# Kernel tuning notes

Measured on AMD Instinct MI355X. Metric: run time of the kernel, lower is better.

## Reference

```python
import jax, jax.numpy as jnp
import numpy as np


def setup_inputs() -> dict:
    key = jax.random.key(0)
    k1, k2, k3 = jax.random.split(key, 3)
    B, V, J = 32, 100000, 52
    vertices = jax.random.normal(k1, (1, V, 3), dtype=jnp.float32)
    lbs_weights = jax.random.uniform(k2, (1, V, J), dtype=jnp.float32)
    skinning_transforms = jax.random.normal(k3, (B, J, 4, 4), dtype=jnp.float32)
    return {
        "vertices": vertices,
        "lbs_weights": lbs_weights,
        "skinning_transforms": skinning_transforms,
    }


def reference(vertices, lbs_weights, skinning_transforms):
    # 3D-vertices branch of Skinning.forward
    B = skinning_transforms.shape[0]
    J = skinning_transforms.shape[1]
    V = vertices.shape[1]
    # W: [B,V,J] (broadcast of [1,V,J]); T_flat: [B,V,16] -> T: [B,V,4,4]
    T = jnp.einsum(
        "bvj,bjx->bvx",
        jnp.broadcast_to(lbs_weights, (B, V, J)),
        skinning_transforms.reshape(B, J, 16),
    ).reshape(B, V, 4, 4)
    # homogeneous vertex coords [B,V,4]
    v_posed_homo = jnp.concatenate(
        [
            jnp.broadcast_to(vertices, (B, V, 3)),
            jnp.ones((B, V, 1), dtype=vertices.dtype),
        ],
        axis=2,
    )
    # per-vertex 4x4 @ 4 transform, keep xyz
    v_homo = jnp.einsum("bvij,bvj->bvi", T, v_posed_homo)
    return v_homo[:, :, :3]
```

## Files before the change

kernel.cpp:

```cpp
#include <hip/hip_runtime.h>
#include <hip/hip_bf16.h>


typedef __attribute__((ext_vector_type(8))) short bf16x8;
typedef __attribute__((ext_vector_type(4))) float f32x4;

constexpr int J      = 52;
constexpr int KSTEPS = 7;
constexpr int NT     = 6;
constexpr int WAVES  = 4;
constexpr int MT     = 2;
constexpr int VPW    = MT * 16;
constexpr int VPB    = WAVES * VPW;

constexpr int SLOTS_FULL = 6 * NT * 64;
constexpr int SLOTS_S6   = NT * 32;
constexpr int ZSLOT      = SLOTS_FULL + SLOTS_S6;
constexpr int NSLOT      = ZSLOT + 1;
constexpr int S6_BASE_B  = SLOTS_FULL * 16;
constexpr int Z_B        = ZSLOT * 16;
constexpr int LDS_B      = 40960;
constexpr int SL_B       = 16 * VPW * 3 * 4;

typedef const __attribute__((address_space(1))) char* gas1_t;
typedef __attribute__((address_space(3))) char* las3_t;

__device__ __forceinline__ unsigned pk2(float a, float b) {
    __hip_bfloat162 h = __float22bfloat162_rn(make_float2(a, b));
    return *reinterpret_cast<unsigned*>(&h);
}

__global__ __launch_bounds__(256) void pack_A(
    const float* __restrict__ xf,
    bf16x8* __restrict__ Bp)
{
    const int slot = blockIdx.x * 256 + threadIdx.x;
    if (slot >= NSLOT) return;

    if (slot == ZSLOT) {
        union { bf16x8 v; unsigned w[4]; } z;
        z.w[0] = z.w[1] = z.w[2] = z.w[3] = 0u;
        Bp[slot] = z.v;
        return;
    }

    int s, t, l;
    if (slot < SLOTS_FULL) {
        s = slot / (NT * 64);
        const int rem = slot - s * (NT * 64);
        t = rem >> 6;
        l = rem & 63;
    } else {
        s = 6;
        const int rem = slot - SLOTS_FULL;
        t = rem >> 5;
        l = rem & 31;
    }
    const int lgrp = l >> 4;
    const int lrow = l & 15;
    const int n = t * 16 + lrow;
    const int b = n / 3;
    const int i = n - 3 * b;
    const int j0 = s * 8 + lgrp * 2;

    const float4* __restrict__ xf4 = reinterpret_cast<const float4*>(xf);
    const float4 m0 = xf4[(b * J + j0) * 4 + i];
    const float4 m1 = xf4[(b * J + j0 + 1) * 4 + i];
    union { bf16x8 v; unsigned w[4]; } r;
    r.w[0] = pk2(m0.x, m0.y); r.w[1] = pk2(m0.z, m0.w);
    r.w[2] = pk2(m1.x, m1.y); r.w[3] = pk2(m1.z, m1.w);
    Bp[slot] = r.v;
}

__global__ __launch_bounds__(256, 4) void skin_mfma(
    const float* __restrict__ verts,
    const float* __restrict__ weights,
    const bf16x8* __restrict__ Bp,
    float* __restrict__ out,
    int V)
{
    __shared__ __align__(16) char sBp[LDS_B];

    const int tid  = threadIdx.x;
    const int lane = tid & 63;
    const int wid  = tid >> 6;
    const int lgrp = lane >> 4;
    const int lrow = lane & 15;
    const int v0   = blockIdx.x * VPB;
    const int v0w  = v0 + wid * VPW;

    {
        const char* g = (const char*)Bp;
        for (int p = wid; p < LDS_B / 1024; p += WAVES) {
            __builtin_amdgcn_global_load_lds(
                (gas1_t)(g + p * 1024 + lane * 16),
                (las3_t)(sBp + p * 1024), 16, 0, 0);
        }
    }

    float hx[MT], hy[MT], hz[MT];
    float2 wv[MT][KSTEPS];
#pragma unroll
    for (int mt = 0; mt < MT; ++mt) {
        const int v   = v0w + mt * 16 + lrow;
        const int vcl = (v < V) ? v : (V - 1);
        hx[mt] = verts[3 * (size_t)vcl + 0];
        hy[mt] = verts[3 * (size_t)vcl + 1];
        hz[mt] = verts[3 * (size_t)vcl + 2];
        const float* wr = weights + (size_t)vcl * J;
#pragma unroll
        for (int s = 0; s < KSTEPS; ++s) {
            const int j0 = s * 8 + lgrp * 2;
            wv[mt][s] = (j0 < J) ? *(const float2*)(wr + j0) : float2{0.f, 0.f};
        }
    }

    __syncthreads();

    f32x4 acc[MT][NT];
#pragma unroll
    for (int mt = 0; mt < MT; ++mt)
#pragma unroll
        for (int t = 0; t < NT; ++t)
            acc[mt][t] = f32x4{0.f, 0.f, 0.f, 0.f};

#pragma unroll
    for (int s = 0; s < KSTEPS; ++s) {
        bf16x8 frag[NT];
#pragma unroll
        for (int t = 0; t < NT; ++t) {
            if (s < 6) {
                frag[t] = *(const bf16x8*)(sBp + ((s * NT + t) * 64 + lane) * 16);
            } else {
                const char* p = (lane < 32)
                    ? (sBp + S6_BASE_B + (t * 32 + lane) * 16)
                    : (sBp + Z_B);
                frag[t] = *(const bf16x8*)p;
            }
        }
#pragma unroll
        for (int mt = 0; mt < MT; ++mt) {
            const float w0 = wv[mt][s].x, w1 = wv[mt][s].y;
            union { bf16x8 v; unsigned w[4]; } xf8;
            xf8.w[0] = pk2(w0 * hx[mt], w0 * hy[mt]);
            xf8.w[1] = pk2(w0 * hz[mt], w0);
            xf8.w[2] = pk2(w1 * hx[mt], w1 * hy[mt]);
            xf8.w[3] = pk2(w1 * hz[mt], w1);
#pragma unroll
            for (int t = 0; t < NT; ++t) {
                acc[mt][t] = __builtin_amdgcn_mfma_f32_16x16x32_bf16(
                    frag[t], xf8.v, acc[mt][t], 0, 0, 0);
            }
        }
    }

    __syncthreads();

    char* const sl = sBp + wid * SL_B;
    const long long validf = ((long long)V - v0w) * 3;
#pragma unroll
    for (int h = 0; h < 2; ++h) {
#pragma unroll
        for (int mt = 0; mt < MT; ++mt) {
            const int vloc = mt * 16 + lrow;
#pragma unroll
            for (int tt = 0; tt < 3; ++tt) {
                const int t = 3 * h + tt;
#pragma unroll
                for (int r = 0; r < 4; ++r) {
                    const int n  = 16 * t + lgrp * 4 + r;
                    const int b  = n / 3;
                    const int i  = n - 3 * b;
                    const int fl = ((b - 16 * h) * VPW + vloc) * 3 + i;
                    *(float*)(sl + fl * 4) = acc[mt][t][r];
                }
            }
        }
        asm volatile("s_waitcnt lgkmcnt(0)" ::: "memory");
        __builtin_amdgcn_sched_barrier(0);

        f32x4 vals[6];
#pragma unroll
        for (int q = 0; q < 6; ++q) {
            const int f = q * 64 + lane;
            vals[q] = *(const f32x4*)(sl + f * 16);
        }
        asm volatile("s_waitcnt lgkmcnt(0)" ::: "memory");
        __builtin_amdgcn_sched_barrier(0);

#pragma unroll
        for (int q = 0; q < 6; ++q) {
            const int f  = q * 64 + lane;
            const int bl = f / 24;
            const int rr = f - bl * 24;
            float* dst = out + (size_t)(16 * h + bl) * (size_t)V * 3
                             + (size_t)v0w * 3 + rr * 4;
            if ((long long)(rr + 1) * 4 <= validf) {
                *(float4*)dst = *(const float4*)&vals[q];
            } else if ((long long)rr * 4 < validf) {
#pragma unroll
                for (int e = 0; e < 4; ++e)
                    if ((long long)(rr * 4 + e) < validf) dst[e] = vals[q][e];
            }
        }
    }
}

extern "C" void kernel_launch(void* const* d_in, const int* in_sizes, int n_in,
                              void* d_out, int out_size, void* d_ws, size_t ws_size,
                              hipStream_t stream)
{
    const float* verts   = (const float*)d_in[0];
    const float* weights = (const float*)d_in[1];
    const float* xf      = (const float*)d_in[2];
    float* out = (float*)d_out;

    const int V = in_sizes[0] / 3;
    bf16x8* Bp = (bf16x8*)d_ws;

    pack_A<<<(NSLOT + 255) / 256, 256, 0, stream>>>(xf, Bp);
    const int nblocks = (V + VPB - 1) / VPB;
    skin_mfma<<<nblocks, 256, 0, stream>>>(verts, weights, Bp, out, V);
}
```

Baseline: 23.84 us.

## Split LDS staging of packed transforms and pad epilogue scratch rows

The LDS fill of packed transform fragments is split in two. Only the first three K-steps' data is awaited before compute starts, and the remainder loads asynchronously while the first MFMA steps run, with an extra barrier before the later steps. The epilogue scratch layout is also padded from 96 to 100 floats per batch row to reduce LDS bank conflicts on the transposing stores. This adds a barrier and changes LDS addressing, and the padded scratch region per wave grows to 6400 bytes, which still fits within the LDS buffer.

```diff
diff --git a/kernel.cpp b/kernel.cpp
--- a/kernel.cpp
+++ b/kernel.cpp
@@ -6,12 +6,12 @@
 typedef __attribute__((ext_vector_type(4))) float f32x4;
 
 constexpr int J      = 52;
-constexpr int KSTEPS = 7;
 constexpr int NT     = 6;
 constexpr int WAVES  = 4;
 constexpr int MT     = 2;
 constexpr int VPW    = MT * 16;
 constexpr int VPB    = WAVES * VPW;
+constexpr int KSTEPS = 7;
 
 constexpr int SLOTS_FULL = 6 * NT * 64;
 constexpr int SLOTS_S6   = NT * 32;
@@ -20,7 +20,9 @@
 constexpr int S6_BASE_B  = SLOTS_FULL * 16;
 constexpr int Z_B        = ZSLOT * 16;
 constexpr int LDS_B      = 40960;
-constexpr int SL_B       = 16 * VPW * 3 * 4;
+constexpr int H1_B       = 3 * NT * 64 * 16;
+constexpr int SPAD       = 100;
+constexpr int SL_B       = 16 * SPAD * 4;
 
 typedef const __attribute__((address_space(1))) char* gas1_t;
 typedef __attribute__((address_space(3))) char* las3_t;
@@ -91,7 +93,7 @@
 
     {
         const char* g = (const char*)Bp;
-        for (int p = wid; p < LDS_B / 1024; p += WAVES) {
+        for (int p = wid; p < H1_B / 1024; p += WAVES) {
             __builtin_amdgcn_global_load_lds(
                 (gas1_t)(g + p * 1024 + lane * 16),
                 (las3_t)(sBp + p * 1024), 16, 0, 0);
@@ -117,6 +119,15 @@
 
     __syncthreads();
 
+    {
+        const char* g = (const char*)Bp;
+        for (int p = H1_B / 1024 + wid; p < LDS_B / 1024; p += WAVES) {
+            __builtin_amdgcn_global_load_lds(
+                (gas1_t)(g + p * 1024 + lane * 16),
+                (las3_t)(sBp + p * 1024), 16, 0, 0);
+        }
+    }
+
     f32x4 acc[MT][NT];
 #pragma unroll
     for (int mt = 0; mt < MT; ++mt)
@@ -125,7 +136,30 @@
             acc[mt][t] = f32x4{0.f, 0.f, 0.f, 0.f};
 
 #pragma unroll
-    for (int s = 0; s < KSTEPS; ++s) {
+    for (int s = 0; s < 3; ++s) {
+        bf16x8 frag[NT];
+#pragma unroll
+        for (int t = 0; t < NT; ++t)
+            frag[t] = *(const bf16x8*)(sBp + ((s * NT + t) * 64 + lane) * 16);
+#pragma unroll
+        for (int mt = 0; mt < MT; ++mt) {
+            const float w0 = wv[mt][s].x, w1 = wv[mt][s].y;
+            union { bf16x8 v; unsigned w[4]; } xf8;
+            xf8.w[0] = pk2(w0 * hx[mt], w0 * hy[mt]);
+            xf8.w[1] = pk2(w0 * hz[mt], w0);
+            xf8.w[2] = pk2(w1 * hx[mt], w1 * hy[mt]);
+            xf8.w[3] = pk2(w1 * hz[mt], w1);
+#pragma unroll
+            for (int t = 0; t < NT; ++t)
+                acc[mt][t] = __builtin_amdgcn_mfma_f32_16x16x32_bf16(
+                    frag[t], xf8.v, acc[mt][t], 0, 0, 0);
+        }
+    }
+
+    __syncthreads();
+
+#pragma unroll
+    for (int s = 3; s < KSTEPS; ++s) {
         bf16x8 frag[NT];
 #pragma unroll
         for (int t = 0; t < NT; ++t) {
@@ -147,10 +181,9 @@
             xf8.w[2] = pk2(w1 * hx[mt], w1 * hy[mt]);
             xf8.w[3] = pk2(w1 * hz[mt], w1);
 #pragma unroll
-            for (int t = 0; t < NT; ++t) {
+            for (int t = 0; t < NT; ++t)
                 acc[mt][t] = __builtin_amdgcn_mfma_f32_16x16x32_bf16(
                     frag[t], xf8.v, acc[mt][t], 0, 0, 0);
-            }
         }
     }
 
@@ -171,7 +204,7 @@
                     const int n  = 16 * t + lgrp * 4 + r;
                     const int b  = n / 3;
                     const int i  = n - 3 * b;
-                    const int fl = ((b - 16 * h) * VPW + vloc) * 3 + i;
+                    const int fl = (b - 16 * h) * SPAD + vloc * 3 + i;
                     *(float*)(sl + fl * 4) = acc[mt][t][r];
                 }
             }
@@ -182,8 +215,10 @@
         f32x4 vals[6];
 #pragma unroll
         for (int q = 0; q < 6; ++q) {
-            const int f = q * 64 + lane;
-            vals[q] = *(const f32x4*)(sl + f * 16);
+            const int f  = q * 64 + lane;
+            const int bl = f / 24;
+            const int rr = f - bl * 24;
+            vals[q] = *(const f32x4*)(sl + bl * (SPAD * 4) + rr * 16);
         }
         asm volatile("s_waitcnt lgkmcnt(0)" ::: "memory");
         __builtin_amdgcn_sched_barrier(0);
```

After: 24.05 us. About the same (+0.9%).
